# Performance work log

Measured on AMD Instinct MI355X. Metric: run time of the kernel, lower is better.

Reference implementation:

```python
import jax, jax.numpy as jnp
import numpy as np


def setup_inputs() -> dict:
    key = jax.random.key(0)
    k1, k2, k3, k4 = jax.random.split(key, 4)
    B, T, C, H = 4, 2048, 1024, 64
    x = jax.random.normal(k1, (B, T, C), dtype=jnp.float32)
    # Linear(embed_dim, head_size, bias=False) weights, stored as [C, H] for x @ W
    s = 1.0 / np.sqrt(C)
    Wq = jax.random.normal(k2, (C, H), dtype=jnp.float32) * s
    Wk = jax.random.normal(k3, (C, H), dtype=jnp.float32) * s
    Wv = jax.random.normal(k4, (C, H), dtype=jnp.float32) * s
    return {"x": x, "Wq": Wq, "Wk": Wk, "Wv": Wv}


def reference(x, Wq, Wk, Wv):
    B, T, C = x.shape
    q = x @ Wq  # [B, T, H]
    k = x @ Wk
    v = x @ Wv
    # NOTE: original scales by embed_dim**-0.5 (C), not head_size**-0.5
    scale = C ** (-0.5)
    wei = jnp.einsum("bqh,bkh->bqk", q, k) * scale  # [B, T, T]
    causal = jnp.tril(jnp.ones((T, T), dtype=bool))
    wei = jnp.where(causal, wei, -jnp.inf)
    wei = jax.nn.softmax(wei, axis=-1)
    # dropout_rate = 0 -> identity
    out = jnp.einsum("bqk,bkh->bqh", wei, v)  # [B, T, H]
    return out
```

## Files before the change

kernel.cpp:

```cpp
#include <hip/hip_runtime.h>
#include <cmath>

#define B_ 4
#define T_ 2048
#define C_ 1024
#define H_ 64
#define SCALE_ 0.03125f
#define NEG_ -3.0e38f

typedef __attribute__((ext_vector_type(4))) float f32x4;
typedef __attribute__((ext_vector_type(8))) short s16x8;
typedef __attribute__((ext_vector_type(4))) unsigned short u16x4;

__device__ inline unsigned short f2bf(float f) {
    union { float f; unsigned u; } v; v.f = f;
    unsigned r = v.u + 0x7FFFu + ((v.u >> 16) & 1u);
    return (unsigned short)(r >> 16);
}

#define LDK 72

__global__ __launch_bounds__(256) void proj_mfma(
    const float* __restrict__ x, const float* __restrict__ Wq,
    const float* __restrict__ Wk, const float* __restrict__ Wv,
    unsigned short* __restrict__ qb, unsigned short* __restrict__ kb,
    unsigned short* __restrict__ vt)
{
    __shared__ unsigned short As[64 * LDK];
    __shared__ unsigned short Bs[64 * LDK];

    const int t = threadIdx.x;
    const int lane = t & 63;
    const int w = t >> 6;
    const int blk = blockIdx.x;
    const int mat = blk % 3;
    const int row0 = (blk / 3) * 64;

    const float* W = (mat == 0) ? Wq : (mat == 1) ? Wk : Wv;

    const int wr = (w >> 1) * 32;
    const int wc = (w & 1) * 32;
    const int fr = lane & 15;
    const int ko = (lane >> 4) * 8;

    f32x4 acc[2][2];
    #pragma unroll
    for (int mi = 0; mi < 2; ++mi)
        #pragma unroll
        for (int ni = 0; ni < 2; ++ni)
            acc[mi][ni] = (f32x4){0.f, 0.f, 0.f, 0.f};

    const int bcol = t & 63;
    const int bkg  = (t >> 6) * 4;

    for (int kt = 0; kt < C_; kt += 64) {
        __syncthreads();
        #pragma unroll
        for (int i = 0; i < 4; ++i) {
            int idx = t + i * 256;
            int r = idx >> 4, kc = (idx & 15) * 4;
            f32x4 xv = *(const f32x4*)(x + (size_t)(row0 + r) * C_ + kt + kc);
            u16x4 bv;
            bv.x = f2bf(xv.x); bv.y = f2bf(xv.y); bv.z = f2bf(xv.z); bv.w = f2bf(xv.w);
            *(u16x4*)&As[r * LDK + kc] = bv;
        }
        #pragma unroll
        for (int i = 0; i < 4; ++i) {
            int kk0 = bkg + i * 16;
            u16x4 bv;
            bv.x = f2bf(W[(size_t)(kt + kk0 + 0) * H_ + bcol]);
            bv.y = f2bf(W[(size_t)(kt + kk0 + 1) * H_ + bcol]);
            bv.z = f2bf(W[(size_t)(kt + kk0 + 2) * H_ + bcol]);
            bv.w = f2bf(W[(size_t)(kt + kk0 + 3) * H_ + bcol]);
            *(u16x4*)&Bs[bcol * LDK + kk0] = bv;
        }
        __syncthreads();
        #pragma unroll
        for (int ks = 0; ks < 2; ++ks) {
            s16x8 a0 = *(const s16x8*)&As[(wr + fr) * LDK + ks * 32 + ko];
            s16x8 a1 = *(const s16x8*)&As[(wr + 16 + fr) * LDK + ks * 32 + ko];
            s16x8 b0 = *(const s16x8*)&Bs[(wc + fr) * LDK + ks * 32 + ko];
            s16x8 b1 = *(const s16x8*)&Bs[(wc + 16 + fr) * LDK + ks * 32 + ko];
            acc[0][0] = __builtin_amdgcn_mfma_f32_16x16x32_bf16(a0, b0, acc[0][0], 0, 0, 0);
            acc[0][1] = __builtin_amdgcn_mfma_f32_16x16x32_bf16(a0, b1, acc[0][1], 0, 0, 0);
            acc[1][0] = __builtin_amdgcn_mfma_f32_16x16x32_bf16(a1, b0, acc[1][0], 0, 0, 0);
            acc[1][1] = __builtin_amdgcn_mfma_f32_16x16x32_bf16(a1, b1, acc[1][1], 0, 0, 0);
        }
    }

    if (mat < 2) {
        unsigned short* outb = (mat == 0) ? qb : kb;
        #pragma unroll
        for (int mi = 0; mi < 2; ++mi)
            #pragma unroll
            for (int ni = 0; ni < 2; ++ni)
                #pragma unroll
                for (int j = 0; j < 4; ++j) {
                    int row = row0 + wr + mi * 16 + (lane >> 4) * 4 + j;
                    int col = wc + ni * 16 + fr;
                    outb[(size_t)row * H_ + col] = f2bf(acc[mi][ni][j]);
                }
    } else {
        __syncthreads();
        #pragma unroll
        for (int mi = 0; mi < 2; ++mi)
            #pragma unroll
            for (int ni = 0; ni < 2; ++ni)
                #pragma unroll
                for (int j = 0; j < 4; ++j) {
                    int r = wr + mi * 16 + (lane >> 4) * 4 + j;
                    int cc = wc + ni * 16 + fr;
                    As[cc * LDK + r] = f2bf(acc[mi][ni][j]);
                }
        __syncthreads();
        int h = t >> 2, c0 = (t & 3) * 16;
        int bb = row0 >> 11, trow = row0 & 2047;
        s16x8 v0 = *(const s16x8*)&As[h * LDK + c0];
        s16x8 v1 = *(const s16x8*)&As[h * LDK + c0 + 8];
        size_t dst = (size_t)bb * H_ * T_ + (size_t)h * T_ + trow + c0;
        *(s16x8*)&vt[dst] = v0;
        *(s16x8*)&vt[dst + 8] = v1;
    }
}

__global__ __launch_bounds__(512, 4) void attn_mfma(
    const unsigned short* __restrict__ qb, const unsigned short* __restrict__ kb,
    const unsigned short* __restrict__ vt, float* __restrict__ out)
{
    __shared__ alignas(16) unsigned short Ps[8][1024];
    __shared__ float Os[8][16][68];
    __shared__ float Mm[8][16];
    __shared__ float Ll[8][16];

    const int t = threadIdx.x, lane = t & 63, w = t >> 6;
    const int fr = lane & 15, hi4 = lane >> 4;
    const int blk = blockIdx.x;
    const int b = blk & 3;
    const int qt = 127 - (blk >> 2);
    const int qbase = qt * 16;

    const unsigned short* qp = qb + ((size_t)b * T_ + qbase) * H_;
    const unsigned short* kp = kb + (size_t)b * T_ * H_;
    const unsigned short* vp = vt + (size_t)b * H_ * T_;

    s16x8 qf0 = *(const s16x8*)&qp[fr * H_ + hi4 * 8];
    s16x8 qf1 = *(const s16x8*)&qp[fr * H_ + 32 + hi4 * 8];

    const int nt = (qbase + 79) >> 6;
    const int per = (nt + 7) >> 3;
    const int tb = w * per;
    int te = tb + per; if (te > nt) te = nt;

    float m[4], l[4];
    f32x4 o[4];
    #pragma unroll
    for (int j = 0; j < 4; ++j) { m[j] = NEG_; l[j] = 0.f; }
    #pragma unroll
    for (int hf = 0; hf < 4; ++hf) o[hf] = (f32x4){0.f, 0.f, 0.f, 0.f};

    unsigned short* P = &Ps[w][0];

    for (int kt = tb; kt < te; ++kt) {
        const int kt0 = kt << 6;

        f32x4 s[4];
        #pragma unroll
        for (int n = 0; n < 4; ++n) {
            const unsigned short* kr = &kp[(size_t)(kt0 + n * 16 + fr) * H_ + hi4 * 8];
            s16x8 kf0 = *(const s16x8*)kr;
            s16x8 kf1 = *(const s16x8*)(kr + 32);
            f32x4 a = (f32x4){0.f, 0.f, 0.f, 0.f};
            a = __builtin_amdgcn_mfma_f32_16x16x32_bf16(qf0, kf0, a, 0, 0, 0);
            a = __builtin_amdgcn_mfma_f32_16x16x32_bf16(qf1, kf1, a, 0, 0, 0);
            s[n] = a;
        }

        if (kt0 + 63 > qbase) {
            #pragma unroll
            for (int n = 0; n < 4; ++n)
                #pragma unroll
                for (int j = 0; j < 4; ++j) {
                    float sv = s[n][j] * SCALE_;
                    s[n][j] = (kt0 + n * 16 + fr > qbase + hi4 * 4 + j) ? NEG_ : sv;
                }
        } else {
            #pragma unroll
            for (int n = 0; n < 4; ++n)
                #pragma unroll
                for (int j = 0; j < 4; ++j) s[n][j] *= SCALE_;
        }

        float mx[4];
        #pragma unroll
        for (int j = 0; j < 4; ++j)
            mx[j] = fmaxf(fmaxf(s[0][j], s[1][j]), fmaxf(s[2][j], s[3][j]));
        #pragma unroll
        for (int d = 1; d < 16; d <<= 1)
            #pragma unroll
            for (int j = 0; j < 4; ++j) mx[j] = fmaxf(mx[j], __shfl_xor(mx[j], d));

        float corr[4], sum[4];
        #pragma unroll
        for (int j = 0; j < 4; ++j) {
            float mn = fmaxf(m[j], mx[j]);
            corr[j] = __expf(m[j] - mn);
            m[j] = mn; sum[j] = 0.f;
        }
        #pragma unroll
        for (int n = 0; n < 4; ++n)
            #pragma unroll
            for (int j = 0; j < 4; ++j) {
                float p = __expf(s[n][j] - m[j]);
                s[n][j] = p; sum[j] += p;
            }
        #pragma unroll
        for (int d = 1; d < 16; d <<= 1)
            #pragma unroll
            for (int j = 0; j < 4; ++j) sum[j] += __shfl_xor(sum[j], d);
        #pragma unroll
        for (int j = 0; j < 4; ++j) l[j] = l[j] * corr[j] + sum[j];
        #pragma unroll
        for (int hf = 0; hf < 4; ++hf)
            #pragma unroll
            for (int j = 0; j < 4; ++j) o[hf][j] *= corr[j];

        #pragma unroll
        for (int n = 0; n < 4; ++n)
            #pragma unroll
            for (int j = 0; j < 4; ++j) {
                int qq = hi4 * 4 + j, kk = n * 16 + fr;
                P[qq * 64 + (((kk >> 3) ^ (qq & 7)) << 3) + (kk & 7)] = f2bf(s[n][j]);
            }

        s16x8 pa0 = *(const s16x8*)&P[fr * 64 + ((hi4 ^ (fr & 7)) << 3)];
        s16x8 pa1 = *(const s16x8*)&P[fr * 64 + (((4 + hi4) ^ (fr & 7)) << 3)];
        #pragma unroll
        for (int hf = 0; hf < 4; ++hf) {
            const unsigned short* vr = &vp[(size_t)(hf * 16 + fr) * T_ + kt0 + hi4 * 8];
            s16x8 vf0 = *(const s16x8*)vr;
            s16x8 vf1 = *(const s16x8*)(vr + 32);
            o[hf] = __builtin_amdgcn_mfma_f32_16x16x32_bf16(pa0, vf0, o[hf], 0, 0, 0);
            o[hf] = __builtin_amdgcn_mfma_f32_16x16x32_bf16(pa1, vf1, o[hf], 0, 0, 0);
        }
    }

    if (fr == 0) {
        #pragma unroll
        for (int j = 0; j < 4; ++j) {
            Mm[w][hi4 * 4 + j] = m[j];
            Ll[w][hi4 * 4 + j] = l[j];
        }
    }
    #pragma unroll
    for (int hf = 0; hf < 4; ++hf)
        #pragma unroll
        for (int j = 0; j < 4; ++j)
            Os[w][hi4 * 4 + j][hf * 16 + fr] = o[hf][j];
    __syncthreads();

    if (t < 256) {
        int qq = t >> 4, h0 = (t & 15) * 4;
        float M = NEG_;
        #pragma unroll
        for (int s8 = 0; s8 < 8; ++s8) M = fmaxf(M, Mm[s8][qq]);
        float L = 0.f;
        f32x4 r = (f32x4){0.f, 0.f, 0.f, 0.f};
        #pragma unroll
        for (int s8 = 0; s8 < 8; ++s8) {
            float e = __expf(Mm[s8][qq] - M);
            L += Ll[s8][qq] * e;
            f32x4 osv = *(const f32x4*)&Os[s8][qq][h0];
            r.x = fmaf(osv.x, e, r.x);
            r.y = fmaf(osv.y, e, r.y);
            r.z = fmaf(osv.z, e, r.z);
            r.w = fmaf(osv.w, e, r.w);
        }
        float il = 1.0f / L;
        r.x *= il; r.y *= il; r.z *= il; r.w *= il;
        *(f32x4*)&out[((size_t)b * T_ + qbase + qq) * H_ + h0] = r;
    }
}

extern "C" void kernel_launch(void* const* d_in, const int* in_sizes, int n_in,
                              void* d_out, int out_size, void* d_ws, size_t ws_size,
                              hipStream_t stream) {
    const float* x  = (const float*)d_in[0];
    const float* Wq = (const float*)d_in[1];
    const float* Wk = (const float*)d_in[2];
    const float* Wv = (const float*)d_in[3];
    float* outp = (float*)d_out;

    unsigned short* base = (unsigned short*)d_ws;
    unsigned short* qbw = base;
    unsigned short* kbw = base + 524288;
    unsigned short* vtw = base + 1048576;

    proj_mfma<<<(B_ * T_ / 64) * 3, 256, 0, stream>>>(x, Wq, Wk, Wv, qbw, kbw, vtw);
    attn_mfma<<<B_ * (T_ / 16), 512, 0, stream>>>(qbw, kbw, vtw, outp);
}
```

Baseline: 50.09 us.

## Transpose QK^T MFMA so each lane owns one query row, cutting shuffles

The QK^T MFMA operands are swapped so the score tile comes out transposed, and each lane then holds scores for a single query row. Row max and row sum need only two cross-lane shuffles instead of sixteen, and the softmax keeps scalar m/l state per lane. The correction factor is redistributed to the O accumulator layout with one shuffle per row, and P is written to LDS as packed 4-element vectors under a new XOR swizzle. The new swizzle and redistribution add indexing complexity, and a layout mistake there would break correctness.

```diff
diff --git a/kernel.cpp b/kernel.cpp
--- a/kernel.cpp
+++ b/kernel.cpp
@@ -151,14 +151,14 @@
     const int tb = w * per;
     int te = tb + per; if (te > nt) te = nt;
 
-    float m[4], l[4];
+    float m = NEG_, l = 0.f;
     f32x4 o[4];
     #pragma unroll
-    for (int j = 0; j < 4; ++j) { m[j] = NEG_; l[j] = 0.f; }
-    #pragma unroll
     for (int hf = 0; hf < 4; ++hf) o[hf] = (f32x4){0.f, 0.f, 0.f, 0.f};
 
     unsigned short* P = &Ps[w][0];
+    const int swz = (fr & 3) << 4;
+    const int qrow = qbase + fr;
 
     for (int kt = tb; kt < te; ++kt) {
         const int kt0 = kt << 6;
@@ -170,8 +170,8 @@
             s16x8 kf0 = *(const s16x8*)kr;
             s16x8 kf1 = *(const s16x8*)(kr + 32);
             f32x4 a = (f32x4){0.f, 0.f, 0.f, 0.f};
-            a = __builtin_amdgcn_mfma_f32_16x16x32_bf16(qf0, kf0, a, 0, 0, 0);
-            a = __builtin_amdgcn_mfma_f32_16x16x32_bf16(qf1, kf1, a, 0, 0, 0);
+            a = __builtin_amdgcn_mfma_f32_16x16x32_bf16(kf0, qf0, a, 0, 0, 0);
+            a = __builtin_amdgcn_mfma_f32_16x16x32_bf16(kf1, qf1, a, 0, 0, 0);
             s[n] = a;
         }
 
@@ -180,8 +180,9 @@
             for (int n = 0; n < 4; ++n)
                 #pragma unroll
                 for (int j = 0; j < 4; ++j) {
+                    int key = kt0 + n * 16 + hi4 * 4 + j;
                     float sv = s[n][j] * SCALE_;
-                    s[n][j] = (kt0 + n * 16 + fr > qbase + hi4 * 4 + j) ? NEG_ : sv;
+                    s[n][j] = (key > qrow) ? NEG_ : sv;
                 }
         } else {
             #pragma unroll
@@ -190,50 +191,45 @@
                 for (int j = 0; j < 4; ++j) s[n][j] *= SCALE_;
         }
 
-        float mx[4];
-        #pragma unroll
-        for (int j = 0; j < 4; ++j)
-            mx[j] = fmaxf(fmaxf(s[0][j], s[1][j]), fmaxf(s[2][j], s[3][j]));
-        #pragma unroll
-        for (int d = 1; d < 16; d <<= 1)
-            #pragma unroll
-            for (int j = 0; j < 4; ++j) mx[j] = fmaxf(mx[j], __shfl_xor(mx[j], d));
-
-        float corr[4], sum[4];
+        float mx01 = fmaxf(fmaxf(s[0][0], s[0][1]), fmaxf(s[0][2], s[0][3]));
+        float mx23 = fmaxf(fmaxf(s[1][0], s[1][1]), fmaxf(s[1][2], s[1][3]));
+        float mx45 = fmaxf(fmaxf(s[2][0], s[2][1]), fmaxf(s[2][2], s[2][3]));
+        float mx67 = fmaxf(fmaxf(s[3][0], s[3][1]), fmaxf(s[3][2], s[3][3]));
+        float mx = fmaxf(fmaxf(mx01, mx23), fmaxf(mx45, mx67));
+        mx = fmaxf(mx, __shfl_xor(mx, 16));
+        mx = fmaxf(mx, __shfl_xor(mx, 32));
+
+        float mn = fmaxf(m, mx);
+        float corr = __expf(m - mn);
+        m = mn;
+        float sum = 0.f;
+        #pragma unroll
+        for (int n = 0; n < 4; ++n)
+            #pragma unroll
+            for (int j = 0; j < 4; ++j) {
+                float p = __expf(s[n][j] - mn);
+                s[n][j] = p; sum += p;
+            }
+        sum += __shfl_xor(sum, 16);
+        sum += __shfl_xor(sum, 32);
+        l = l * corr + sum;
+
         #pragma unroll
         for (int j = 0; j < 4; ++j) {
-            float mn = fmaxf(m[j], mx[j]);
-            corr[j] = __expf(m[j] - mn);
-            m[j] = mn; sum[j] = 0.f;
-        }
-        #pragma unroll
-        for (int n = 0; n < 4; ++n)
-            #pragma unroll
-            for (int j = 0; j < 4; ++j) {
-                float p = __expf(s[n][j] - m[j]);
-                s[n][j] = p; sum[j] += p;
-            }
-        #pragma unroll
-        for (int d = 1; d < 16; d <<= 1)
-            #pragma unroll
-            for (int j = 0; j < 4; ++j) sum[j] += __shfl_xor(sum[j], d);
-        #pragma unroll
-        for (int j = 0; j < 4; ++j) l[j] = l[j] * corr[j] + sum[j];
-        #pragma unroll
-        for (int hf = 0; hf < 4; ++hf)
-            #pragma unroll
-            for (int j = 0; j < 4; ++j) o[hf][j] *= corr[j];
-
-        #pragma unroll
-        for (int n = 0; n < 4; ++n)
-            #pragma unroll
-            for (int j = 0; j < 4; ++j) {
-                int qq = hi4 * 4 + j, kk = n * 16 + fr;
-                P[qq * 64 + (((kk >> 3) ^ (qq & 7)) << 3) + (kk & 7)] = f2bf(s[n][j]);
-            }
-
-        s16x8 pa0 = *(const s16x8*)&P[fr * 64 + ((hi4 ^ (fr & 7)) << 3)];
-        s16x8 pa1 = *(const s16x8*)&P[fr * 64 + (((4 + hi4) ^ (fr & 7)) << 3)];
+            float cj = __shfl(corr, (lane & 48) + hi4 * 4 + j);
+            o[0][j] *= cj; o[1][j] *= cj; o[2][j] *= cj; o[3][j] *= cj;
+        }
+
+        #pragma unroll
+        for (int n = 0; n < 4; ++n) {
+            u16x4 pk;
+            pk.x = f2bf(s[n][0]); pk.y = f2bf(s[n][1]);
+            pk.z = f2bf(s[n][2]); pk.w = f2bf(s[n][3]);
+            *(u16x4*)&P[fr * 64 + ((n * 16 + hi4 * 4) ^ swz)] = pk;
+        }
+        s16x8 pa0 = *(const s16x8*)&P[fr * 64 + ((hi4 * 8) ^ swz)];
+        s16x8 pa1 = *(const s16x8*)&P[fr * 64 + ((32 + hi4 * 8) ^ swz)];
+
         #pragma unroll
         for (int hf = 0; hf < 4; ++hf) {
             const unsigned short* vr = &vp[(size_t)(hf * 16 + fr) * T_ + kt0 + hi4 * 8];
@@ -244,13 +240,7 @@
         }
     }
 
-    if (fr == 0) {
-        #pragma unroll
-        for (int j = 0; j < 4; ++j) {
-            Mm[w][hi4 * 4 + j] = m[j];
-            Ll[w][hi4 * 4 + j] = l[j];
-        }
-    }
+    if (hi4 == 0) { Mm[w][fr] = m; Ll[w][fr] = l; }
     #pragma unroll
     for (int hf = 0; hf < 4; ++hf)
         #pragma unroll
```

Measured after the change: 49.57 us. No clear change (-1.0%).
